# Kernel tuning notes

Hardware: AMD Instinct MI355X
Metric: run time of the kernel (lower is better)

## Reference

```python
import jax, jax.numpy as jnp
import numpy as np

D_MODEL = 1024
N_HEADS = 16
DEPTH = D_MODEL // N_HEADS
B, S = 2, 2048


def setup_inputs() -> dict:
    key = jax.random.key(0)
    ks = jax.random.split(key, 11)
    scale = 1.0 / np.sqrt(D_MODEL)
    return {
        "q": jax.random.normal(ks[0], (B, S, D_MODEL), jnp.float32),
        "k": jax.random.normal(ks[1], (B, S, D_MODEL), jnp.float32),
        "v": jax.random.normal(ks[2], (B, S, D_MODEL), jnp.float32),
        "wq": jax.random.normal(ks[3], (D_MODEL, D_MODEL), jnp.float32) * scale,
        "bq": jnp.zeros((D_MODEL,), jnp.float32),
        "wk": jax.random.normal(ks[4], (D_MODEL, D_MODEL), jnp.float32) * scale,
        "bk": jnp.zeros((D_MODEL,), jnp.float32),
        "wv": jax.random.normal(ks[5], (D_MODEL, D_MODEL), jnp.float32) * scale,
        "bv": jnp.zeros((D_MODEL,), jnp.float32),
        "wo": jax.random.normal(ks[6], (D_MODEL, D_MODEL), jnp.float32) * scale,
        "bo": jnp.zeros((D_MODEL,), jnp.float32),
    }


def _mha(q, k, v, wq, bq, wk, bk, wv, bv, wo, bo):
    b, s, _ = q.shape
    # separate QKV projections
    qh = (q @ wq + bq).reshape(b, s, N_HEADS, DEPTH).transpose(0, 2, 1, 3)  # [b,h,s,d]
    kh = (k @ wk + bk).reshape(b, s, N_HEADS, DEPTH).transpose(0, 2, 1, 3)
    vh = (v @ wv + bv).reshape(b, s, N_HEADS, DEPTH).transpose(0, 2, 1, 3)
    # keras.layers.Attention default: UNSCALED dot-product scores, causal mask
    scores = jnp.einsum("bhqd,bhkd->bhqk", qh, kh)  # [b,h,s,s]
    causal = jnp.tril(jnp.ones((s, s), bool))
    scores = jnp.where(causal, scores, jnp.float32(-1e9))
    attn = jax.nn.softmax(scores, axis=-1)
    out = jnp.einsum("bhqk,bhkd->bhqd", attn, vh)  # [b,h,s,d]
    out = out.transpose(0, 2, 1, 3).reshape(b, s, D_MODEL)
    return out @ wo + bo


def reference(q, k, v, wq, bq, wk, bk, wv, bv, wo, bo):
    return _mha(q, k, v, wq, bq, wk, bk, wv, bv, wo, bo)
```

## Files before the change

### kernel.cpp

```cpp
#include <hip/hip_runtime.h>
#include <stdint.h>

#define AS1q __attribute__((address_space(1)))
#define AS3q __attribute__((address_space(3)))

typedef unsigned short US;
typedef __bf16 bf16x8 __attribute__((ext_vector_type(8)));
typedef float f32x4 __attribute__((ext_vector_type(4)));
typedef float f32x16 __attribute__((ext_vector_type(16)));
typedef float f32x2 __attribute__((ext_vector_type(2)));
typedef __bf16 bf16x2 __attribute__((ext_vector_type(2)));

#define LOG2E 1.44269504088896340736f

__device__ __forceinline__ US f2bf(float f) {
  union { float f; uint32_t u; } c; c.f = f;
  uint32_t u = c.u;
  return (US)((u + 0x7fffu + ((u >> 16) & 1u)) >> 16);
}

__device__ __forceinline__ bf16x8 asb(uint4 u) {
  union { uint4 u; bf16x8 b; } c; c.u = u; return c.b;
}

__device__ __forceinline__ uint32_t pk2(float a, float b) {
  f32x2 fv; fv[0] = a; fv[1] = b;
  bf16x2 bb = __builtin_convertvector(fv, bf16x2);
  union { bf16x2 b; uint32_t u; } c; c.b = bb; return c.u;
}

__device__ __forceinline__ void gload16(const void* g, void* l) {
  __builtin_amdgcn_global_load_lds((AS1q void*)(void*)g, (AS3q void*)l, 16, 0, 0);
}

__global__ void prep_kernel(const float* __restrict__ q, const float* __restrict__ k,
                            const float* __restrict__ v,
                            const float* __restrict__ w0, const float* __restrict__ w1,
                            const float* __restrict__ w2, const float* __restrict__ w3,
                            US* __restrict__ qb, US* __restrict__ kb, US* __restrict__ vb,
                            US* __restrict__ t0, US* __restrict__ t1,
                            US* __restrict__ t2, US* __restrict__ t3) {
  __shared__ US T[64 * 68];
  const int bx = blockIdx.x;
  const int t = threadIdx.x;
  if (bx < 6144) {
    const int ten = bx >> 11, chunk = bx & 2047;
    const float* s; US* d;
    if (ten == 0)      { s = q; d = qb; }
    else if (ten == 1) { s = k; d = kb; }
    else               { s = v; d = vb; }
    int i = (chunk * 256 + t) * 8;
    float4 f0 = *(const float4*)&s[i];
    float4 f1 = *(const float4*)&s[i + 4];
    ushort4 u0, u1;
    u0.x = f2bf(f0.x); u0.y = f2bf(f0.y); u0.z = f2bf(f0.z); u0.w = f2bf(f0.w);
    u1.x = f2bf(f1.x); u1.y = f2bf(f1.y); u1.z = f2bf(f1.z); u1.w = f2bf(f1.w);
    *(ushort4*)&d[i] = u0;
    *(ushort4*)&d[i + 4] = u1;
    return;
  }
  const int idx = bx - 6144;
  const int wsel = idx >> 8, rem = idx & 255;
  const int n0 = (rem & 15) * 64, k0 = (rem >> 4) * 64;
  const float* W; US* Wt;
  if (wsel == 0)      { W = w0; Wt = t0; }
  else if (wsel == 1) { W = w1; Wt = t1; }
  else if (wsel == 2) { W = w2; Wt = t2; }
  else                { W = w3; Wt = t3; }
#pragma unroll
  for (int it = 0; it < 4; ++it) {
    int p = t + it * 256;
    int row = p >> 4, c4 = (p & 15) * 4;
    float4 f = *(const float4*)&W[(k0 + row) * 1024 + n0 + c4];
    ushort4 u;
    u.x = f2bf(f.x); u.y = f2bf(f.y); u.z = f2bf(f.z); u.w = f2bf(f.w);
    *(ushort4*)&T[row * 68 + c4] = u;
  }
  __syncthreads();
#pragma unroll
  for (int it = 0; it < 4; ++it) {
    int p = t + it * 256;
    int rn = p >> 4, ck = (p & 15) * 4;
    ushort4 o;
    o.x = T[(ck + 0) * 68 + rn];
    o.y = T[(ck + 1) * 68 + rn];
    o.z = T[(ck + 2) * 68 + rn];
    o.w = T[(ck + 3) * 68 + rn];
    *(ushort4*)&Wt[(n0 + rn) * 1024 + k0 + ck] = o;
  }
}

template <bool SWAP>
__device__ __forceinline__ void gemm_core64(const US* A, const US* Wt,
                                            int m0, int n0, US* As, US* Bs,
                                            f32x4 acc[4][4]) {
  const int tid = threadIdx.x;
  const int wave = tid >> 6, lane = tid & 63;
  const int quad = lane >> 4, l16 = lane & 15;
  const int wm = wave >> 1, wn = wave & 1;
#pragma unroll
  for (int i = 0; i < 4; ++i)
#pragma unroll
    for (int j = 0; j < 4; ++j) acc[i][j] = (f32x4)0.0f;

  const int srow = tid >> 3;
  const int sch = (tid & 7) ^ (srow & 7);
  const US* gA = A + (size_t)(m0 + srow) * 1024 + sch * 8;
  const US* gB = Wt + (size_t)(n0 + srow) * 1024 + sch * 8;
  US* lA = As + wave * 512;
  US* lB = Bs + wave * 512;

  for (int k0 = 0; k0 < 1024; k0 += 64) {
#pragma unroll
    for (int c = 0; c < 4; ++c) {
      gload16(gA + (size_t)c * 32 * 1024 + k0, lA + c * 2048);
      gload16(gB + (size_t)c * 32 * 1024 + k0, lB + c * 2048);
    }
    __syncthreads();
    uint4 af[4][2], bf_[4][2];
#pragma unroll
    for (int mt = 0; mt < 4; ++mt) {
      const int row = wm * 64 + mt * 16 + l16;
      af[mt][0] = *(const uint4*)&As[row * 64 + ((quad ^ (row & 7)) << 3)];
      af[mt][1] = *(const uint4*)&As[row * 64 + (((4 + quad) ^ (row & 7)) << 3)];
    }
#pragma unroll
    for (int nt = 0; nt < 4; ++nt) {
      const int row = wn * 64 + nt * 16 + l16;
      bf_[nt][0] = *(const uint4*)&Bs[row * 64 + ((quad ^ (row & 7)) << 3)];
      bf_[nt][1] = *(const uint4*)&Bs[row * 64 + (((4 + quad) ^ (row & 7)) << 3)];
    }
#pragma unroll
    for (int i = 0; i < 4; ++i)
#pragma unroll
      for (int j = 0; j < 4; ++j) {
        if (SWAP) {
          acc[i][j] = __builtin_amdgcn_mfma_f32_16x16x32_bf16(asb(bf_[i][0]), asb(af[j][0]),
                                                              acc[i][j], 0, 0, 0);
          acc[i][j] = __builtin_amdgcn_mfma_f32_16x16x32_bf16(asb(bf_[i][1]), asb(af[j][1]),
                                                              acc[i][j], 0, 0, 0);
        } else {
          acc[i][j] = __builtin_amdgcn_mfma_f32_16x16x32_bf16(asb(af[i][0]), asb(bf_[j][0]),
                                                              acc[i][j], 0, 0, 0);
          acc[i][j] = __builtin_amdgcn_mfma_f32_16x16x32_bf16(asb(af[i][1]), asb(bf_[j][1]),
                                                              acc[i][j], 0, 0, 0);
        }
      }
    __syncthreads();
  }
}

__global__ __launch_bounds__(256, 4) void gemm_qkv_kernel(
    const US* __restrict__ qb, const US* __restrict__ kb, const US* __restrict__ vb,
    const US* __restrict__ wfT,
    const float* __restrict__ bq, const float* __restrict__ bk, const float* __restrict__ bv,
    US* __restrict__ qh, US* __restrict__ kh, US* __restrict__ vt) {
  __shared__ __align__(16) US As[8192], Bs[8192];
  const int m0 = blockIdx.x * 128, n0 = blockIdx.y * 128;
  const int which = n0 >> 10;
  const int nl0 = n0 & 1023;
  const US* A = (which == 0) ? qb : (which == 1) ? kb : vb;
  const float* bias = (which == 0) ? bq : (which == 1) ? bk : bv;
  const int tid = threadIdx.x, wave = tid >> 6, lane = tid & 63;
  const int quad = lane >> 4, l16 = lane & 15;
  const int wm = wave >> 1, wn = wave & 1;
  f32x4 acc[4][4];
  if (which == 2) {
    gemm_core64<true>(A, wfT, m0, n0, As, Bs, acc);
#pragma unroll
    for (int nt = 0; nt < 4; ++nt) {
      int dg = nl0 + wn * 64 + nt * 16 + quad * 4;
#pragma unroll
      for (int r = 0; r < 4; ++r) {
        int d = dg + r;
        float bval = bias[d];
        int hh = d >> 6, dd = d & 63;
#pragma unroll
        for (int mt = 0; mt < 4; ++mt) {
          int sg = m0 + wm * 64 + mt * 16;
          int bb = sg >> 11, ss = sg & 2047;
          vt[(((size_t)bb * 16 + hh) * 64 + dd) * 2048 + ss + l16] =
              f2bf(acc[nt][mt][r] + bval);
        }
      }
    }
  } else {
    gemm_core64<false>(A, wfT, m0, n0, As, Bs, acc);
    US* O = (which == 0) ? qh : kh;
    const float scale = (which == 0) ? LOG2E : 1.0f;
#pragma unroll
    for (int nt = 0; nt < 4; ++nt) {
      int nl = nl0 + wn * 64 + nt * 16 + l16;
      float bval = bias[nl];
      int hh = nl >> 6, d = nl & 63;
#pragma unroll
      for (int mt = 0; mt < 4; ++mt) {
#pragma unroll
        for (int r = 0; r < 4; ++r) {
          int m = m0 + wm * 64 + mt * 16 + quad * 4 + r;
          int bb = m >> 11, s = m & 2047;
          O[((bb * 16 + hh) * 2048 + s) * 64 + d] = f2bf((acc[mt][nt][r] + bval) * scale);
        }
      }
    }
  }
}

__global__ __launch_bounds__(256, 4) void gemm_out_kernel(
    const US* __restrict__ ao, const US* __restrict__ woT,
    const float* __restrict__ bo, float* __restrict__ out) {
  __shared__ __align__(16) US As[8192], Bs[4096];
  const int m0 = blockIdx.x * 128, n0 = blockIdx.y * 64;
  const int tid = threadIdx.x;
  const int wave = tid >> 6, lane = tid & 63;
  const int quad = lane >> 4, l16 = lane & 15;
  f32x4 acc[2][4];
#pragma unroll
  for (int i = 0; i < 2; ++i)
#pragma unroll
    for (int j = 0; j < 4; ++j) acc[i][j] = (f32x4)0.0f;

  const int srow = tid >> 3;
  const int sch = (tid & 7) ^ (srow & 7);
  const US* gA = ao + (size_t)(m0 + srow) * 1024 + sch * 8;
  const US* gB = woT + (size_t)(n0 + srow) * 1024 + sch * 8;
  US* lA = As + wave * 512;
  US* lB = Bs + wave * 512;

  for (int k0 = 0; k0 < 1024; k0 += 64) {
#pragma unroll
    for (int c = 0; c < 4; ++c)
      gload16(gA + (size_t)c * 32 * 1024 + k0, lA + c * 2048);
#pragma unroll
    for (int c = 0; c < 2; ++c)
      gload16(gB + (size_t)c * 32 * 1024 + k0, lB + c * 2048);
    __syncthreads();
    uint4 af[2][2], bf_[4][2];
#pragma unroll
    for (int mt = 0; mt < 2; ++mt) {
      const int row = wave * 32 + mt * 16 + l16;
      af[mt][0] = *(const uint4*)&As[row * 64 + ((quad ^ (row & 7)) << 3)];
      af[mt][1] = *(const uint4*)&As[row * 64 + (((4 + quad) ^ (row & 7)) << 3)];
    }
#pragma unroll
    for (int nt = 0; nt < 4; ++nt) {
      const int row = nt * 16 + l16;
      bf_[nt][0] = *(const uint4*)&Bs[row * 64 + ((quad ^ (row & 7)) << 3)];
      bf_[nt][1] = *(const uint4*)&Bs[row * 64 + (((4 + quad) ^ (row & 7)) << 3)];
    }
#pragma unroll
    for (int mt = 0; mt < 2; ++mt)
#pragma unroll
      for (int nt = 0; nt < 4; ++nt) {
        acc[mt][nt] = __builtin_amdgcn_mfma_f32_16x16x32_bf16(asb(af[mt][0]), asb(bf_[nt][0]),
                                                              acc[mt][nt], 0, 0, 0);
        acc[mt][nt] = __builtin_amdgcn_mfma_f32_16x16x32_bf16(asb(af[mt][1]), asb(bf_[nt][1]),
                                                              acc[mt][nt], 0, 0, 0);
      }
    __syncthreads();
  }
#pragma unroll
  for (int nt = 0; nt < 4; ++nt) {
    int n = n0 + nt * 16 + l16;
    float bval = bo[n];
#pragma unroll
    for (int mt = 0; mt < 2; ++mt) {
#pragma unroll
      for (int r = 0; r < 4; ++r) {
        int m = m0 + wave * 32 + mt * 16 + quad * 4 + r;
        out[m * 1024 + n] = acc[mt][nt][r] + bval;
      }
    }
  }
}

__global__ __launch_bounds__(512, 2) void attn_kernel(
    const US* __restrict__ qh, const US* __restrict__ kh,
    const US* __restrict__ vt, US* __restrict__ aout) {
  __shared__ __align__(16) char arena[73728];
  US* KsA = (US*)arena;
  US* VsA = (US*)(arena + 32768);
  US* Qs  = (US*)(arena + 65536);
  float* Oex = (float*)arena;
  float* lEx = (float*)(arena + 69632);

  const int tid = threadIdx.x;
  const int wave = tid >> 6, lane = tid & 63;
  const int l31 = lane & 31, lh = lane >> 5;
  const int w_m = wave & 1, w_k = wave >> 1;
  const int bh = blockIdx.x;
  const int b = bh >> 4, h = bh & 15;
  const int jg = blockIdx.y;

  const US* gkb = kh + (size_t)bh * 2048 * 64;
  const US* gvb = vt + (size_t)bh * 64 * 2048;

  for (int ei = 0; ei < 2; ++ei) {
    const int qt = ei ? jg : (31 - jg);
    const int q0 = qt * 64;
    const int nit = (qt >> 1) + 1;
    __syncthreads();
    {
      const US* gq = qh + ((size_t)bh * 2048 + q0) * 64;
      {
        int p = tid;
        int row = p >> 3, c = (p & 7) ^ (row & 7);
        gload16(gq + row * 64 + c * 8, Qs + wave * 512);
      }
#pragma unroll
      for (int ro = 0; ro < 2; ++ro) {
        int p = tid + ro * 512;
        int row = p >> 3, c = (p & 7) ^ (row & 7);
        gload16(gkb + row * 64 + c * 8, KsA + ro * 4096 + wave * 512);
      }
#pragma unroll
      for (int ro = 0; ro < 2; ++ro) {
        int p = tid + ro * 512;
        int row = p >> 4, c = (p & 15) ^ (row & 15);
        gload16(gvb + row * 2048 + c * 8, VsA + ro * 4096 + wave * 512);
      }
    }
    __syncthreads();

    const int qrow = w_m * 32 + l31;
    uint4 bq[4];
#pragma unroll
    for (int s = 0; s < 4; ++s)
      bq[s] = *(const uint4*)&Qs[qrow * 64 + (((2 * s + lh) ^ (qrow & 7)) * 8)];
    const int q_g = q0 + qrow;

    float l_lane = 0.0f;
    f32x16 Oa0 = (f32x16)0.0f, Oa1 = (f32x16)0.0f;

    for (int it = 0; it < nit; ++it) {
      const int cb = it & 1;
      const int kb = it * 128;
      if (it) __syncthreads();
      if (it + 1 < nit) {
        const US* gk = gkb + (kb + 128) * 64;
        const US* gv = gvb + (kb + 128);
        US* kd = KsA + (cb ^ 1) * 8192;
        US* vd = VsA + (cb ^ 1) * 8192;
#pragma unroll
        for (int ro = 0; ro < 2; ++ro) {
          int p = tid + ro * 512;
          int row = p >> 3, c = (p & 7) ^ (row & 7);
          gload16(gk + row * 64 + c * 8, kd + ro * 4096 + wave * 512);
        }
#pragma unroll
        for (int ro = 0; ro < 2; ++ro) {
          int p = tid + ro * 512;
          int row = p >> 4, c = (p & 15) ^ (row & 15);
          gload16(gv + row * 2048 + c * 8, vd + ro * 4096 + wave * 512);
        }
      }
      const US* Kc = KsA + cb * 8192;
      const US* Vc = VsA + cb * 8192;

      f32x16 sa0 = (f32x16)0.0f;
      const int kr0 = w_k * 32 + l31;
#pragma unroll
      for (int s = 0; s < 4; ++s) {
        uint4 ka0 = *(const uint4*)&Kc[kr0 * 64 + (((2 * s + lh) ^ (kr0 & 7)) * 8)];
        sa0 = __builtin_amdgcn_mfma_f32_32x32x16_bf16(asb(ka0), asb(bq[s]), sa0, 0, 0, 0);
      }

      const bool diag = (it == nit - 1);
      float e[16];
      const int kbase = kb + w_k * 32 + 4 * lh;
#pragma unroll
      for (int r = 0; r < 16; ++r) {
        float ev = __builtin_amdgcn_exp2f(sa0[r]);
        if (diag) {
          int key_g = kbase + (r & 3) + 8 * (r >> 2);
          if (key_g > q_g) ev = 0.0f;
        }
        e[r] = ev;
        l_lane += ev;
      }

#pragma unroll
      for (int s2 = 0; s2 < 2; ++s2) {
        uint32_t PA0 = pk2(e[8 * s2 + 0], e[8 * s2 + 1]);
        uint32_t PA1 = pk2(e[8 * s2 + 2], e[8 * s2 + 3]);
        uint32_t PB0 = pk2(e[8 * s2 + 4], e[8 * s2 + 5]);
        uint32_t PB1 = pk2(e[8 * s2 + 6], e[8 * s2 + 7]);
        uint32_t W0 = (uint32_t)__shfl_xor((int)(lh ? PA0 : PB0), 32, 64);
        uint32_t W1 = (uint32_t)__shfl_xor((int)(lh ? PA1 : PB1), 32, 64);
        uint4 bp;
        bp.x = lh ? W0 : PA0;
        bp.y = lh ? W1 : PA1;
        bp.z = lh ? PB0 : W0;
        bp.w = lh ? PB1 : W1;
        const int c_log = w_k * 4 + s2 * 2 + lh;
        int vr0 = l31;
        uint4 va0 = *(const uint4*)&Vc[vr0 * 128 + ((c_log ^ (vr0 & 15)) * 8)];
        Oa0 = __builtin_amdgcn_mfma_f32_32x32x16_bf16(asb(va0), asb(bp), Oa0, 0, 0, 0);
        int vr1 = 32 + l31;
        uint4 va1 = *(const uint4*)&Vc[vr1 * 128 + ((c_log ^ (vr1 & 15)) * 8)];
        Oa1 = __builtin_amdgcn_mfma_f32_32x32x16_bf16(asb(va1), asb(bp), Oa1, 0, 0, 0);
      }
    }

    float l_q = l_lane + __shfl_xor(l_lane, 32, 64);

    __syncthreads();
    {
      float* myO = Oex + w_k * (64 * 68);
      int q_idx = w_m * 32 + l31;
#pragma unroll
      for (int r = 0; r < 16; ++r) {
        int dr = 4 * lh + (r & 3) + 8 * (r >> 2);
        myO[q_idx * 68 + dr] = Oa0[r];
        myO[q_idx * 68 + 32 + dr] = Oa1[r];
      }
      if (lh == 0) lEx[w_k * 64 + q_idx] = l_q;
    }
    __syncthreads();
    {
      int q_idx = tid >> 3;
      int dseg = (tid & 7) * 8;
      float inv = 1.0f / (lEx[q_idx] + lEx[64 + q_idx] + lEx[128 + q_idx] + lEx[192 + q_idx]);
      union { US s[8]; uint4 v; } ob;
#pragma unroll
      for (int t2 = 0; t2 < 8; ++t2) {
        float o = Oex[q_idx * 68 + dseg + t2]
                + Oex[64 * 68 + q_idx * 68 + dseg + t2]
                + Oex[2 * 64 * 68 + q_idx * 68 + dseg + t2]
                + Oex[3 * 64 * 68 + q_idx * 68 + dseg + t2];
        ob.s[t2] = f2bf(o * inv);
      }
      US* dst = aout + ((size_t)b * 2048 + q0 + q_idx) * 1024 + h * 64 + dseg;
      *(uint4*)dst = ob.v;
    }
  }
}

extern "C" void kernel_launch(void* const* d_in, const int* in_sizes, int n_in,
                              void* d_out, int out_size, void* d_ws, size_t ws_size,
                              hipStream_t stream) {
  const float* q  = (const float*)d_in[0];
  const float* k  = (const float*)d_in[1];
  const float* v  = (const float*)d_in[2];
  const float* wq = (const float*)d_in[3];
  const float* bq = (const float*)d_in[4];
  const float* wk = (const float*)d_in[5];
  const float* bk = (const float*)d_in[6];
  const float* wv = (const float*)d_in[7];
  const float* bv = (const float*)d_in[8];
  const float* wo = (const float*)d_in[9];
  const float* bo = (const float*)d_in[10];
  float* out = (float*)d_out;

  char* ws = (char*)d_ws;
  const size_t MB = 1024 * 1024;
  US* qb  = (US*)(ws + 0 * MB);
  US* kb  = (US*)(ws + 8 * MB);
  US* vb  = (US*)(ws + 16 * MB);
  US* wqT = (US*)(ws + 24 * MB);
  US* wkT = (US*)(ws + 26 * MB);
  US* wvT = (US*)(ws + 28 * MB);
  US* woT = (US*)(ws + 30 * MB);
  US* qh  = (US*)(ws + 32 * MB);
  US* kh  = (US*)(ws + 40 * MB);
  US* vt  = (US*)(ws + 48 * MB);
  US* ao  = (US*)(ws + 56 * MB);

  prep_kernel<<<7168, 256, 0, stream>>>(q, k, v, wq, wk, wv, wo,
                                        qb, kb, vb, wqT, wkT, wvT, woT);
  gemm_qkv_kernel<<<dim3(32, 24), 256, 0, stream>>>(qb, kb, vb, wqT,
                                                    bq, bk, bv, qh, kh, vt);
  attn_kernel<<<dim3(32, 16), 512, 0, stream>>>(qh, kh, vt, ao);
  gemm_out_kernel<<<dim3(32, 16), 256, 0, stream>>>(ao, woT, bo, out);
}
```

Before: 199.6 us.

## Single-buffer attention LDS to raise occupancy, use permlane32 swap for P

```diff
diff --git a/kernel.cpp b/kernel.cpp
--- a/kernel.cpp
+++ b/kernel.cpp
@@ -10,6 +10,7 @@
 typedef float f32x16 __attribute__((ext_vector_type(16)));
 typedef float f32x2 __attribute__((ext_vector_type(2)));
 typedef __bf16 bf16x2 __attribute__((ext_vector_type(2)));
+typedef int v2i __attribute__((ext_vector_type(2)));
 
 #define LOG2E 1.44269504088896340736f
 
@@ -31,6 +32,11 @@
 
 __device__ __forceinline__ void gload16(const void* g, void* l) {
   __builtin_amdgcn_global_load_lds((AS1q void*)(void*)g, (AS3q void*)l, 16, 0, 0);
+}
+
+__device__ __forceinline__ void plswap(uint32_t& a, uint32_t& b) {
+  v2i r = __builtin_amdgcn_permlane32_swap((int)a, (int)b, false, false);
+  a = (uint32_t)r[0]; b = (uint32_t)r[1];
 }
 
 __global__ void prep_kernel(const float* __restrict__ q, const float* __restrict__ k,
@@ -274,15 +280,15 @@
   }
 }
 
-__global__ __launch_bounds__(512, 2) void attn_kernel(
+__global__ __launch_bounds__(512, 8) void attn_kernel(
     const US* __restrict__ qh, const US* __restrict__ kh,
     const US* __restrict__ vt, US* __restrict__ aout) {
-  __shared__ __align__(16) char arena[73728];
-  US* KsA = (US*)arena;
-  US* VsA = (US*)(arena + 32768);
-  US* Qs  = (US*)(arena + 65536);
+  __shared__ __align__(16) char arena[40960];
+  US* Ks = (US*)arena;
+  US* Vs = (US*)(arena + 16384);
+  US* Qs = (US*)(arena + 32768);
   float* Oex = (float*)arena;
-  float* lEx = (float*)(arena + 69632);
+  float* lEx = (float*)(arena + 34816);
 
   const int tid = threadIdx.x;
   const int wave = tid >> 6, lane = tid & 63;
@@ -302,132 +308,123 @@
     __syncthreads();
     {
       const US* gq = qh + ((size_t)bh * 2048 + q0) * 64;
-      {
-        int p = tid;
-        int row = p >> 3, c = (p & 7) ^ (row & 7);
-        gload16(gq + row * 64 + c * 8, Qs + wave * 512);
-      }
-#pragma unroll
-      for (int ro = 0; ro < 2; ++ro) {
-        int p = tid + ro * 512;
-        int row = p >> 3, c = (p & 7) ^ (row & 7);
-        gload16(gkb + row * 64 + c * 8, KsA + ro * 4096 + wave * 512);
-      }
-#pragma unroll
-      for (int ro = 0; ro < 2; ++ro) {
-        int p = tid + ro * 512;
-        int row = p >> 4, c = (p & 15) ^ (row & 15);
-        gload16(gvb + row * 2048 + c * 8, VsA + ro * 4096 + wave * 512);
-      }
-    }
-    __syncthreads();
-
+      int row = tid >> 3, c = (tid & 7) ^ (row & 7);
+      gload16(gq + row * 64 + c * 8, Qs + wave * 512);
+    }
     const int qrow = w_m * 32 + l31;
-    uint4 bq[4];
-#pragma unroll
-    for (int s = 0; s < 4; ++s)
-      bq[s] = *(const uint4*)&Qs[qrow * 64 + (((2 * s + lh) ^ (qrow & 7)) * 8)];
     const int q_g = q0 + qrow;
 
     float l_lane = 0.0f;
     f32x16 Oa0 = (f32x16)0.0f, Oa1 = (f32x16)0.0f;
 
     for (int it = 0; it < nit; ++it) {
-      const int cb = it & 1;
       const int kb = it * 128;
-      if (it) __syncthreads();
-      if (it + 1 < nit) {
-        const US* gk = gkb + (kb + 128) * 64;
-        const US* gv = gvb + (kb + 128);
-        US* kd = KsA + (cb ^ 1) * 8192;
-        US* vd = VsA + (cb ^ 1) * 8192;
+      {
+        const US* gk = gkb + (size_t)kb * 64;
+        const US* gv = gvb + kb;
 #pragma unroll
         for (int ro = 0; ro < 2; ++ro) {
           int p = tid + ro * 512;
           int row = p >> 3, c = (p & 7) ^ (row & 7);
-          gload16(gk + row * 64 + c * 8, kd + ro * 4096 + wave * 512);
+          gload16(gk + row * 64 + c * 8, Ks + ro * 4096 + wave * 512);
         }
 #pragma unroll
         for (int ro = 0; ro < 2; ++ro) {
           int p = tid + ro * 512;
           int row = p >> 4, c = (p & 15) ^ (row & 15);
-          gload16(gv + row * 2048 + c * 8, vd + ro * 4096 + wave * 512);
-        }
-      }
-      const US* Kc = KsA + cb * 8192;
-      const US* Vc = VsA + cb * 8192;
+          gload16(gv + row * 2048 + c * 8, Vs + ro * 4096 + wave * 512);
+        }
+      }
+      __syncthreads();
 
       f32x16 sa0 = (f32x16)0.0f;
       const int kr0 = w_k * 32 + l31;
 #pragma unroll
       for (int s = 0; s < 4; ++s) {
-        uint4 ka0 = *(const uint4*)&Kc[kr0 * 64 + (((2 * s + lh) ^ (kr0 & 7)) * 8)];
-        sa0 = __builtin_amdgcn_mfma_f32_32x32x16_bf16(asb(ka0), asb(bq[s]), sa0, 0, 0, 0);
+        uint4 bq = *(const uint4*)&Qs[qrow * 64 + (((2 * s + lh) ^ (qrow & 7)) * 8)];
+        uint4 ka = *(const uint4*)&Ks[kr0 * 64 + (((2 * s + lh) ^ (kr0 & 7)) * 8)];
+        sa0 = __builtin_amdgcn_mfma_f32_32x32x16_bf16(asb(ka), asb(bq), sa0, 0, 0, 0);
       }
 
       const bool diag = (it == nit - 1);
-      float e[16];
       const int kbase = kb + w_k * 32 + 4 * lh;
 #pragma unroll
-      for (int r = 0; r < 16; ++r) {
-        float ev = __builtin_amdgcn_exp2f(sa0[r]);
-        if (diag) {
-          int key_g = kbase + (r & 3) + 8 * (r >> 2);
-          if (key_g > q_g) ev = 0.0f;
-        }
-        e[r] = ev;
-        l_lane += ev;
-      }
-
-#pragma unroll
       for (int s2 = 0; s2 < 2; ++s2) {
-        uint32_t PA0 = pk2(e[8 * s2 + 0], e[8 * s2 + 1]);
-        uint32_t PA1 = pk2(e[8 * s2 + 2], e[8 * s2 + 3]);
-        uint32_t PB0 = pk2(e[8 * s2 + 4], e[8 * s2 + 5]);
-        uint32_t PB1 = pk2(e[8 * s2 + 6], e[8 * s2 + 7]);
-        uint32_t W0 = (uint32_t)__shfl_xor((int)(lh ? PA0 : PB0), 32, 64);
-        uint32_t W1 = (uint32_t)__shfl_xor((int)(lh ? PA1 : PB1), 32, 64);
-        uint4 bp;
-        bp.x = lh ? W0 : PA0;
-        bp.y = lh ? W1 : PA1;
-        bp.z = lh ? PB0 : W0;
-        bp.w = lh ? PB1 : W1;
+        float e[8];
+#pragma unroll
+        for (int j = 0; j < 8; ++j) {
+          float ev = __builtin_amdgcn_exp2f(sa0[8 * s2 + j]);
+          if (diag) {
+            int key_g = kbase + (j & 3) + 16 * s2 + 8 * (j >> 2);
+            if (key_g > q_g) ev = 0.0f;
+          }
+          e[j] = ev;
+          l_lane += ev;
+        }
+        uint32_t x0 = pk2(e[0], e[1]);
+        uint32_t y0 = pk2(e[2], e[3]);
+        uint32_t z0 = pk2(e[4], e[5]);
+        uint32_t w0 = pk2(e[6], e[7]);
+        plswap(x0, z0);
+        plswap(y0, w0);
+        uint4 bp; bp.x = x0; bp.y = y0; bp.z = z0; bp.w = w0;
         const int c_log = w_k * 4 + s2 * 2 + lh;
-        int vr0 = l31;
-        uint4 va0 = *(const uint4*)&Vc[vr0 * 128 + ((c_log ^ (vr0 & 15)) * 8)];
+        uint4 va0 = *(const uint4*)&Vs[l31 * 128 + ((c_log ^ (l31 & 15)) * 8)];
         Oa0 = __builtin_amdgcn_mfma_f32_32x32x16_bf16(asb(va0), asb(bp), Oa0, 0, 0, 0);
-        int vr1 = 32 + l31;
-        uint4 va1 = *(const uint4*)&Vc[vr1 * 128 + ((c_log ^ (vr1 & 15)) * 8)];
+        uint4 va1 = *(const uint4*)&Vs[(32 + l31) * 128 + ((c_log ^ ((32 + l31) & 15)) * 8)];
         Oa1 = __builtin_amdgcn_mfma_f32_32x32x16_bf16(asb(va1), asb(bp), Oa1, 0, 0, 0);
       }
+      __syncthreads();
     }
 
     float l_q = l_lane + __shfl_xor(l_lane, 32, 64);
 
-    __syncthreads();
     {
-      float* myO = Oex + w_k * (64 * 68);
       int q_idx = w_m * 32 + l31;
-#pragma unroll
-      for (int r = 0; r < 16; ++r) {
-        int dr = 4 * lh + (r & 3) + 8 * (r >> 2);
-        myO[q_idx * 68 + dr] = Oa0[r];
-        myO[q_idx * 68 + 32 + dr] = Oa1[r];
+      if (w_k < 2) {
+        float* myO = Oex + w_k * (64 * 68);
+#pragma unroll
+        for (int r = 0; r < 16; ++r) {
+          int dr = 4 * lh + (r & 3) + 8 * (r >> 2);
+          myO[q_idx * 68 + dr] = Oa0[r];
+          myO[q_idx * 68 + 32 + dr] = Oa1[r];
+        }
       }
       if (lh == 0) lEx[w_k * 64 + q_idx] = l_q;
     }
     __syncthreads();
+    float po[8];
+    float inv;
     {
       int q_idx = tid >> 3;
       int dseg = (tid & 7) * 8;
-      float inv = 1.0f / (lEx[q_idx] + lEx[64 + q_idx] + lEx[128 + q_idx] + lEx[192 + q_idx]);
+      inv = 1.0f / (lEx[q_idx] + lEx[64 + q_idx] + lEx[128 + q_idx] + lEx[192 + q_idx]);
+#pragma unroll
+      for (int t2 = 0; t2 < 8; ++t2)
+        po[t2] = Oex[q_idx * 68 + dseg + t2] + Oex[64 * 68 + q_idx * 68 + dseg + t2];
+    }
+    __syncthreads();
+    {
+      int q_idx = w_m * 32 + l31;
+      if (w_k >= 2) {
+        float* myO = Oex + (w_k - 2) * (64 * 68);
+#pragma unroll
+        for (int r = 0; r < 16; ++r) {
+          int dr = 4 * lh + (r & 3) + 8 * (r >> 2);
+          myO[q_idx * 68 + dr] = Oa0[r];
+          myO[q_idx * 68 + 32 + dr] = Oa1[r];
+        }
+      }
+    }
+    __syncthreads();
+    {
+      int q_idx = tid >> 3;
+      int dseg = (tid & 7) * 8;
       union { US s[8]; uint4 v; } ob;
 #pragma unroll
       for (int t2 = 0; t2 < 8; ++t2) {
-        float o = Oex[q_idx * 68 + dseg + t2]
-                + Oex[64 * 68 + q_idx * 68 + dseg + t2]
-                + Oex[2 * 64 * 68 + q_idx * 68 + dseg + t2]
-                + Oex[3 * 64 * 68 + q_idx * 68 + dseg + t2];
+        float o = po[t2] + Oex[q_idx * 68 + dseg + t2]
+                + Oex[64 * 68 + q_idx * 68 + dseg + t2];
         ob.s[t2] = f2bf(o * inv);
       }
       US* dst = aout + ((size_t)b * 2048 + q0 + q_idx) * 1024 + h * 64 + dseg;
```

Measured after the change: 414.5 us. 2.08x slower.
